# Kernel optimization log

Measured on AMD Instinct MI355X. Metric: run time of the kernel, lower is better.

Reference implementation:

```python
import jax, jax.numpy as jnp
import numpy as np

IN_CH = 256
QK_CH = IN_CH // 8  # 32

def setup_inputs() -> dict:
    key = jax.random.key(0)
    ks = jax.random.split(key, 7)
    x = jax.random.normal(ks[0], (4, IN_CH, 64, 64), dtype=jnp.float32)
    s_in = 1.0 / np.sqrt(IN_CH)
    # 1x1 conv weights stored as [out_ch, in_ch]; biases [out_ch]
    Wq = jax.random.uniform(ks[1], (QK_CH, IN_CH), jnp.float32, -s_in, s_in)
    bq = jax.random.uniform(ks[2], (QK_CH,), jnp.float32, -s_in, s_in)
    Wk = jax.random.uniform(ks[3], (QK_CH, IN_CH), jnp.float32, -s_in, s_in)
    bk = jax.random.uniform(ks[4], (QK_CH,), jnp.float32, -s_in, s_in)
    Wv = jax.random.uniform(ks[5], (IN_CH, IN_CH), jnp.float32, -s_in, s_in)
    bv = jax.random.uniform(ks[6], (IN_CH,), jnp.float32, -s_in, s_in)
    return {"x": x, "Wq": Wq, "bq": bq, "Wk": Wk, "bk": bk, "Wv": Wv, "bv": bv}

def reference(x, Wq, bq, Wk, bk, Wv, bv):
    n, c, h, w = x.shape
    xf = x.reshape(n, c, h * w)  # [n, c, hw]
    # 1x1 convs == per-position channel matmuls
    q = jnp.einsum('oc,ncs->nos', Wq, xf) + bq[None, :, None]  # [n, c/8, hw]
    k = jnp.einsum('oc,ncs->nos', Wk, xf) + bk[None, :, None]  # [n, c/8, hw]
    v = jnp.einsum('oc,ncs->nos', Wv, xf) + bv[None, :, None]  # [n, c,  hw]
    # energy[n, i, j] = <q[:, i], k[:, j]>  (no scaling, as in original)
    energy = jnp.einsum('nci,ncj->nij', q, k)  # [n, hw, hw]
    attention = jax.nn.softmax(energy, axis=-1)
    # out[n, c, i] = sum_j v[n, c, j] * attention[n, i, j]
    out = jnp.einsum('ncj,nij->nci', v, attention)
    return out.reshape(n, c, h, w)
```

## Files before the change

kernel.cpp:

```cpp
#include <hip/hip_runtime.h>
#include <hip/hip_bf16.h>
#include <stdint.h>
#include <stddef.h>

typedef unsigned short u16;
typedef unsigned int   u32;
typedef __attribute__((ext_vector_type(8))) short bf16x8;
typedef __attribute__((ext_vector_type(4))) float f32x4;

#define LOG2E   1.44269504f
#define EXP_OFF 23.0831206f

static __device__ __forceinline__ float bf2f(u16 v) {
    u32 u = ((u32)v) << 16; float f; __builtin_memcpy(&f, &u, 4); return f;
}
static __device__ __forceinline__ u16 f2bf(float f) {
    u32 u; __builtin_memcpy(&u, &f, 4);
    u32 r = (u + 0x7fffu + ((u >> 16) & 1u)) >> 16; return (u16)r;
}
static __device__ __forceinline__ float as_f(u32 u) { float f; __builtin_memcpy(&f, &u, 4); return f; }
static __device__ __forceinline__ u32   as_u(float f) { u32 u; __builtin_memcpy(&u, &f, 4); return u; }

static __device__ __forceinline__ int detect_f32_wave0(const void* x, int t) {
    const u32* xw = (const u32*)x;
    int bad = 0;
    #pragma unroll
    for (int k = 0; k < 4; ++k) {
        u32 wv = xw[(t << 2) + k];
        int e = (wv >> 7) & 0xff;
        bad += (e >= 160);
    }
    unsigned long long m = __ballot(bad > 0);
    return (__popcll(m) >= 8) ? 1 : 0;
}


__global__ __launch_bounds__(256) void qkv_proj_kernel(
    const void* __restrict__ x,
    const void* __restrict__ Wq, const void* __restrict__ bq,
    const void* __restrict__ Wk, const void* __restrict__ bk,
    const void* __restrict__ Wv, const void* __restrict__ bv,
    u16* __restrict__ qws, u16* __restrict__ kws, u16* __restrict__ vws,
    int n_off)
{
    __shared__ float Ws[32][68];
    __shared__ float Xs[32][68];
    __shared__ int dtf;

    const int t   = threadIdx.x;
    const int it  = blockIdx.x;
    const int ot  = blockIdx.y;
    const int n_w = blockIdx.z;
    const int n_g = n_off + n_w;
    const int i0  = it << 6;
    const int tx  = t & 15;
    const int ty  = t >> 4;

    if (t < 64) { int f = detect_f32_wave0(x, t); if (t == 0) dtf = f; }
    __syncthreads();
    const bool isf32 = (dtf != 0);

    float acc[4][4];
    #pragma unroll
    for (int a = 0; a < 4; ++a)
        #pragma unroll
        for (int b = 0; b < 4; ++b) acc[a][b] = 0.f;

    const int o_st   = t & 63;
    const int kk0    = (t >> 6) << 3;
    const int och_st = (ot << 6) + o_st;
    int wsel, wrow;
    if (och_st < 32)      { wsel = 0; wrow = och_st; }
    else if (och_st < 64) { wsel = 1; wrow = och_st - 32; }
    else                  { wsel = 2; wrow = och_st - 64; }
    const void* wbase = (wsel == 0) ? Wq : (wsel == 1) ? Wk : Wv;

    for (int c0 = 0; c0 < 256; c0 += 32) {
        if (isf32) {
            const float* wf = (const float*)wbase + wrow * 256 + c0 + kk0;
            #pragma unroll
            for (int k8 = 0; k8 < 8; ++k8) Ws[kk0 + k8][o_st] = wf[k8];
            const float* xf = (const float*)x;
            #pragma unroll
            for (int v = 0; v < 2; ++v) {
                int g  = t + (v << 8);
                int kk = g >> 4;
                int ii = (g & 15) << 2;
                float4 x4 = *(const float4*)(xf +
                    (((size_t)(n_g * 256 + c0 + kk)) << 12) + i0 + ii);
                Xs[kk][ii + 0] = x4.x; Xs[kk][ii + 1] = x4.y;
                Xs[kk][ii + 2] = x4.z; Xs[kk][ii + 3] = x4.w;
            }
        } else {
            const u16* wh = (const u16*)wbase + wrow * 256 + c0 + kk0;
            #pragma unroll
            for (int k8 = 0; k8 < 8; ++k8) Ws[kk0 + k8][o_st] = bf2f(wh[k8]);
            const u16* xh = (const u16*)x;
            #pragma unroll
            for (int v = 0; v < 2; ++v) {
                int g  = t + (v << 8);
                int kk = g >> 4;
                int ii = (g & 15) << 2;
                ushort4 u4 = *(const ushort4*)(xh +
                    (((size_t)(n_g * 256 + c0 + kk)) << 12) + i0 + ii);
                Xs[kk][ii + 0] = bf2f(u4.x); Xs[kk][ii + 1] = bf2f(u4.y);
                Xs[kk][ii + 2] = bf2f(u4.z); Xs[kk][ii + 3] = bf2f(u4.w);
            }
        }
        __syncthreads();

        #pragma unroll
        for (int kk = 0; kk < 32; ++kk) {
            float4 a4 = *(const float4*)&Ws[kk][ty << 2];
            float4 b4 = *(const float4*)&Xs[kk][tx << 2];
            float av[4] = {a4.x, a4.y, a4.z, a4.w};
            float bw[4] = {b4.x, b4.y, b4.z, b4.w};
            #pragma unroll
            for (int a = 0; a < 4; ++a)
                #pragma unroll
                for (int b = 0; b < 4; ++b)
                    acc[a][b] += av[a] * bw[b];
        }
        __syncthreads();
    }

    #pragma unroll
    for (int a = 0; a < 4; ++a) {
        int och = (ot << 6) + (ty << 2) + a;
        float bias;
        if (isf32) {
            if (och < 32)      bias = ((const float*)bq)[och];
            else if (och < 64) bias = ((const float*)bk)[och - 32];
            else               bias = ((const float*)bv)[och - 64];
        } else {
            if (och < 32)      bias = bf2f(((const u16*)bq)[och]);
            else if (och < 64) bias = bf2f(((const u16*)bk)[och - 32]);
            else               bias = bf2f(((const u16*)bv)[och - 64]);
        }
        if (och < 32) {
            #pragma unroll
            for (int b = 0; b < 4; ++b) {
                int i = i0 + (tx << 2) + b;
                qws[(((size_t)(n_w << 12) + i) << 5) + och] =
                    f2bf((acc[a][b] + bias) * LOG2E);
            }
        } else if (och < 64) {
            #pragma unroll
            for (int b = 0; b < 4; ++b) {
                int i = i0 + (tx << 2) + b;
                kws[(((size_t)(n_w << 12) + i) << 5) + (och - 32)] =
                    f2bf(acc[a][b] + bias);
            }
        } else {
            const int c = och - 64;
            const int i = i0 + (tx << 2);
            ushort4 h;
            h.x = f2bf(acc[a][0] + bias);
            h.y = f2bf(acc[a][1] + bias);
            h.z = f2bf(acc[a][2] + bias);
            h.w = f2bf(acc[a][3] + bias);
            const size_t addr = ((size_t)n_w << 20)
                + ((size_t)(c >> 4) << 16)
                + ((size_t)(i >> 5) << 9)
                + (size_t)((((((i & 31) >> 3) << 4) + (c & 15)) << 3) + (i & 7));
            *(ushort4*)(vws + addr) = h;
        }
    }
}

__global__ __launch_bounds__(1024) void flash_mfma6(
    const u16* __restrict__ qws, const u16* __restrict__ kws,
    const u16* __restrict__ vws, void* __restrict__ out,
    const void* __restrict__ x, int n_off, int nshift)
{
    __shared__ __align__(16) char arena[17920];
    __shared__ __align__(16) float lS[64];
    __shared__ int dtf;
    u16*   PsA  = (u16*)arena;
    float* Dbuf = (float*)arena;

    const int t    = threadIdx.x;
    const int lane = t & 63;
    const int w    = t >> 6;
    const int n16  = lane & 15;
    const int quad = lane >> 4;
    const int bid  = blockIdx.x;
    const int n_w  = bid & ((1 << nshift) - 1);
    const int qt   = bid >> nshift;
    const int n_g  = n_off + n_w;
    const int i0   = qt << 6;

    if (t < 64) {
        int f = detect_f32_wave0(x, t);
        if (t == 0) dtf = f;
        lS[t] = 0.f;
    }

    const u16* qb = qws + (((size_t)n_w) << 17);
    const u16* kb = kws + (((size_t)n_w) << 17);
    const u16* vb = vws + (((size_t)n_w) << 20);

    const int qsub_s = w & 3;
    const int jsub   = w >> 2;
    const int cq = w & 7;
    const int jq = w >> 3;

    const bf16x8 qfrag =
        *(const bf16x8*)(qb + ((size_t)(i0 + (qsub_s << 4) + n16) << 5) + (quad << 3));

    f32x4 acc[4][2];
    #pragma unroll
    for (int a = 0; a < 4; ++a)
        #pragma unroll
        for (int b = 0; b < 2; ++b) acc[a][b] = (f32x4){0.f, 0.f, 0.f, 0.f};
    float lp[4] = {0.f, 0.f, 0.f, 0.f};

    const int jcol = (jsub << 4) + n16;
    const int j8   = jcol >> 3;
    const int jlo  = jcol & 7;
    const int ksw  = (jq << 2) + quad;

    const u16* vfp0 = vb + ((size_t)(cq << 1) << 16) + ((size_t)jq << 9)
                         + ((size_t)((quad << 4) + n16) << 3);
    const u16* vfp1 = vfp0 + 65536;

    bf16x8 kreg, vf0, vf1;

    kreg = *(const bf16x8*)(kb + ((size_t)((jsub << 4) + n16) << 5) + (quad << 3));
    {
        u16* Ps = PsA;
        const f32x4 z = {0.f, 0.f, 0.f, 0.f};
        f32x4 s = __builtin_amdgcn_mfma_f32_16x16x32_bf16(qfrag, kreg, z, 0, 0, 0);
        #pragma unroll
        for (int r = 0; r < 4; ++r) {
            const int qrow = (qsub_s << 4) + (quad << 2) + r;
            float p = exp2f(s[r] - EXP_OFF);
            u32 u = as_u(p) & 0xffff0000u;
            lp[r] += as_f(u);
            Ps[qrow * 64 + ((j8 ^ (qrow & 7)) << 3) + jlo] = (u16)(u >> 16);
        }
        kreg = *(const bf16x8*)(kb + ((size_t)(64 + (jsub << 4) + n16) << 5) + (quad << 3));
        vf0 = *(const bf16x8*)(vfp0);
        vf1 = *(const bf16x8*)(vfp1);
    }
    __syncthreads();

    for (int tile = 1; tile < 64; ++tile) {
        const int par  = tile & 1;
        u16* Psc = PsA + (par << 12);
        u16* Psp = PsA + ((par ^ 1) << 12);

        bf16x8 pa[4];
        #pragma unroll
        for (int qs = 0; qs < 4; ++qs) {
            const int qrow = (qs << 4) + n16;
            pa[qs] = *(const bf16x8*)&Psp[qrow * 64 + ((ksw ^ (qrow & 7)) << 3)];
        }
        #pragma unroll
        for (int qs = 0; qs < 4; ++qs) {
            acc[qs][0] = __builtin_amdgcn_mfma_f32_16x16x32_bf16(pa[qs], vf0, acc[qs][0], 0, 0, 0);
            acc[qs][1] = __builtin_amdgcn_mfma_f32_16x16x32_bf16(pa[qs], vf1, acc[qs][1], 0, 0, 0);
        }

        vf0 = *(const bf16x8*)(vfp0 + ((size_t)tile << 10));
        vf1 = *(const bf16x8*)(vfp1 + ((size_t)tile << 10));

        const f32x4 z = {0.f, 0.f, 0.f, 0.f};
        f32x4 s = __builtin_amdgcn_mfma_f32_16x16x32_bf16(qfrag, kreg, z, 0, 0, 0);
        #pragma unroll
        for (int r = 0; r < 4; ++r) {
            const int qrow = (qsub_s << 4) + (quad << 2) + r;
            float p = exp2f(s[r] - EXP_OFF);
            u32 u = as_u(p) & 0xffff0000u;
            lp[r] += as_f(u);
            Psc[qrow * 64 + ((j8 ^ (qrow & 7)) << 3) + jlo] = (u16)(u >> 16);
        }

        if (tile < 63) {
            const int j0n = (tile + 1) << 6;
            kreg = *(const bf16x8*)(kb + ((size_t)(j0n + (jsub << 4) + n16) << 5)
                                    + (quad << 3));
        }
        __syncthreads();
    }

    {
        u16* Psp = PsA + (1 << 12);
        bf16x8 pa[4];
        #pragma unroll
        for (int qs = 0; qs < 4; ++qs) {
            const int qrow = (qs << 4) + n16;
            pa[qs] = *(const bf16x8*)&Psp[qrow * 64 + ((ksw ^ (qrow & 7)) << 3)];
        }
        #pragma unroll
        for (int qs = 0; qs < 4; ++qs) {
            acc[qs][0] = __builtin_amdgcn_mfma_f32_16x16x32_bf16(pa[qs], vf0, acc[qs][0], 0, 0, 0);
            acc[qs][1] = __builtin_amdgcn_mfma_f32_16x16x32_bf16(pa[qs], vf1, acc[qs][1], 0, 0, 0);
        }
    }

    #pragma unroll
    for (int r = 0; r < 4; ++r) {
        lp[r] += __shfl_xor(lp[r], 1);
        lp[r] += __shfl_xor(lp[r], 2);
        lp[r] += __shfl_xor(lp[r], 4);
        lp[r] += __shfl_xor(lp[r], 8);
    }
    if (n16 == 0) {
        #pragma unroll
        for (int r = 0; r < 4; ++r)
            atomicAdd(&lS[(qsub_s << 4) + (quad << 2) + r], lp[r]);
    }
    __syncthreads();
    if (t < 64) lS[t] = 1.0f / lS[t];
    const bool isf32 = (dtf != 0);

    for (int chunk = 0; chunk < 4; ++chunk) {
        __syncthreads();
        if (jq == 1 && (cq >> 1) == chunk) {
            #pragma unroll
            for (int qs = 0; qs < 4; ++qs)
                #pragma unroll
                for (int cs = 0; cs < 2; ++cs)
                    *(f32x4*)&Dbuf[(((cq & 1) << 5) + (cs << 4) + n16) * 68 +
                                   (qs << 4) + (quad << 2)] = acc[qs][cs];
        }
        __syncthreads();
        if (jq == 0 && (cq >> 1) == chunk) {
            #pragma unroll
            for (int qs = 0; qs < 4; ++qs)
                #pragma unroll
                for (int cs = 0; cs < 2; ++cs) {
                    float* p = &Dbuf[(((cq & 1) << 5) + (cs << 4) + n16) * 68 +
                                     (qs << 4) + (quad << 2)];
                    f32x4 d = *(f32x4*)p;
                    d += acc[qs][cs];
                    *(f32x4*)p = d;
                }
        }
        __syncthreads();
        const int c_l = t >> 4;
        const int qg  = (t & 15) << 2;
        float4 d  = *(float4*)&Dbuf[c_l * 68 + qg];
        float4 rl = *(float4*)&lS[qg];
        const int c_glob = (chunk << 6) + c_l;
        const size_t ob = (((size_t)(n_g * 256 + c_glob)) << 12) + i0 + qg;
        if (isf32) {
            float4 o = make_float4(d.x * rl.x, d.y * rl.y, d.z * rl.z, d.w * rl.w);
            *(float4*)((float*)out + ob) = o;
        } else {
            union { uint2 v; u16 h[4]; } o;
            o.h[0] = f2bf(d.x * rl.x);
            o.h[1] = f2bf(d.y * rl.y);
            o.h[2] = f2bf(d.z * rl.z);
            o.h[3] = f2bf(d.w * rl.w);
            *(uint2*)((u16*)out + ob) = o.v;
        }
    }
}

extern "C" void kernel_launch(void* const* d_in, const int* in_sizes, int n_in,
                              void* d_out, int out_size, void* d_ws, size_t ws_size,
                              hipStream_t stream)
{
    const void* x  = d_in[0];
    const void* Wq = d_in[1];
    const void* bq = d_in[2];
    const void* Wk = d_in[3];
    const void* bk = d_in[4];
    const void* Wv = d_in[5];
    const void* bv = d_in[6];

    const size_t full_need = (size_t)(4u * 4096u) * (32 + 32 + 256) * 2;
    if (ws_size >= full_need) {
        u16* qws = (u16*)d_ws;
        u16* kws = qws + (size_t)4 * 4096 * 32;
        u16* vws = kws + (size_t)4 * 4096 * 32;
        qkv_proj_kernel<<<dim3(64, 5, 4), dim3(256), 0, stream>>>(
            x, Wq, bq, Wk, bk, Wv, bv, qws, kws, vws, 0);
        flash_mfma6<<<dim3(256), dim3(1024), 0, stream>>>(
            qws, kws, vws, d_out, x, 0, 2);
    } else {
        u16* qws = (u16*)d_ws;
        u16* kws = qws + (size_t)4096 * 32;
        u16* vws = kws + (size_t)4096 * 32;
        for (int n = 0; n < 4; ++n) {
            qkv_proj_kernel<<<dim3(64, 5, 1), dim3(256), 0, stream>>>(
                x, Wq, bq, Wk, bk, Wv, bv, qws, kws, vws, n);
            flash_mfma6<<<dim3(64), dim3(1024), 0, stream>>>(
                qws, kws, vws, d_out, x, n, 0);
        }
    }
}
```

Before: 160.2 us.

## Rewrite QKV projection to use bf16 MFMA with swizzled LDS weights

Replaces the fp32 SIMT tiled GEMM in the QKV projection with a kernel that stages a 64x256 weight slab in LDS as bf16 (XOR-swizzled) and computes with 16x16x32 bf16 MFMA instructions. Activations are loaded straight from global memory per lane, converted to bf16 and prefetched one step ahead. The grid becomes 1D with the batch index in the low bits so that consecutive blocks cover different batches. Rounding inputs to bf16 before the projection lowers precision, and the strided per-lane global loads of x may coalesce less well.

```diff
diff --git a/kernel.cpp b/kernel.cpp
--- a/kernel.cpp
+++ b/kernel.cpp
@@ -35,134 +35,148 @@
 }
 
 
-__global__ __launch_bounds__(256) void qkv_proj_kernel(
+__global__ __launch_bounds__(256) void qkv_proj_mfma(
     const void* __restrict__ x,
     const void* __restrict__ Wq, const void* __restrict__ bq,
     const void* __restrict__ Wk, const void* __restrict__ bk,
     const void* __restrict__ Wv, const void* __restrict__ bv,
     u16* __restrict__ qws, u16* __restrict__ kws, u16* __restrict__ vws,
-    int n_off)
+    int n_off, int nshiftp)
 {
-    __shared__ float Ws[32][68];
-    __shared__ float Xs[32][68];
+    __shared__ u16 Wl[64 * 256];
     __shared__ int dtf;
 
-    const int t   = threadIdx.x;
-    const int it  = blockIdx.x;
-    const int ot  = blockIdx.y;
-    const int n_w = blockIdx.z;
-    const int n_g = n_off + n_w;
-    const int i0  = it << 6;
-    const int tx  = t & 15;
-    const int ty  = t >> 4;
+    const int t    = threadIdx.x;
+    const int bid  = blockIdx.x;
+    const int n_w  = bid & ((1 << nshiftp) - 1);
+    const int rest = bid >> nshiftp;
+    const int g    = rest % 5;
+    const int it   = rest / 5;
+    const int n_g  = n_off + n_w;
+    const int i0   = it << 6;
 
     if (t < 64) { int f = detect_f32_wave0(x, t); if (t == 0) dtf = f; }
     __syncthreads();
     const bool isf32 = (dtf != 0);
 
-    float acc[4][4];
     #pragma unroll
-    for (int a = 0; a < 4; ++a)
-        #pragma unroll
-        for (int b = 0; b < 4; ++b) acc[a][b] = 0.f;
-
-    const int o_st   = t & 63;
-    const int kk0    = (t >> 6) << 3;
-    const int och_st = (ot << 6) + o_st;
-    int wsel, wrow;
-    if (och_st < 32)      { wsel = 0; wrow = och_st; }
-    else if (och_st < 64) { wsel = 1; wrow = och_st - 32; }
-    else                  { wsel = 2; wrow = och_st - 64; }
-    const void* wbase = (wsel == 0) ? Wq : (wsel == 1) ? Wk : Wv;
-
-    for (int c0 = 0; c0 < 256; c0 += 32) {
+    for (int k = 0; k < 16; ++k) {
+        int idx  = t + (k << 8);
+        int row  = idx >> 6;
+        int col4 = (idx & 63) << 2;
+        const void* src; int srow;
+        if (g == 0) {
+            if (row < 32) { src = Wq; srow = row; }
+            else          { src = Wk; srow = row - 32; }
+        } else { src = Wv; srow = ((g - 1) << 6) + row; }
+        ushort4 h;
         if (isf32) {
-            const float* wf = (const float*)wbase + wrow * 256 + c0 + kk0;
-            #pragma unroll
-            for (int k8 = 0; k8 < 8; ++k8) Ws[kk0 + k8][o_st] = wf[k8];
-            const float* xf = (const float*)x;
-            #pragma unroll
-            for (int v = 0; v < 2; ++v) {
-                int g  = t + (v << 8);
-                int kk = g >> 4;
-                int ii = (g & 15) << 2;
-                float4 x4 = *(const float4*)(xf +
-                    (((size_t)(n_g * 256 + c0 + kk)) << 12) + i0 + ii);
-                Xs[kk][ii + 0] = x4.x; Xs[kk][ii + 1] = x4.y;
-                Xs[kk][ii + 2] = x4.z; Xs[kk][ii + 3] = x4.w;
+            float4 wv = *((const float4*)((const float*)src + srow * 256 + col4));
+            h.x = f2bf(wv.x); h.y = f2bf(wv.y); h.z = f2bf(wv.z); h.w = f2bf(wv.w);
+        } else {
+            h = *((const ushort4*)((const u16*)src + srow * 256 + col4));
+        }
+        *(ushort4*)&Wl[(row << 8) + (col4 ^ ((row & 7) << 3))] = h;
+    }
+    __syncthreads();
+
+    const int lane = t & 63;
+    const int w    = t >> 6;
+    const int n16  = lane & 15;
+    const int quad = lane >> 4;
+    const int i_b  = i0 + (w << 4);
+    const int i    = i_b + n16;
+    const int swz  = (n16 & 7) << 3;
+
+    f32x4 acc[4];
+    #pragma unroll
+    for (int f = 0; f < 4; ++f) acc[f] = (f32x4){0.f, 0.f, 0.f, 0.f};
+
+    if (isf32) {
+        const float* xp = (const float*)x
+            + (((size_t)(n_g * 256 + (quad << 3))) << 12) + i;
+        float af[8];
+        #pragma unroll
+        for (int e = 0; e < 8; ++e) af[e] = xp[(size_t)e << 12];
+        #pragma unroll
+        for (int c8 = 0; c8 < 8; ++c8) {
+            bf16x8 a;
+            #pragma unroll
+            for (int e = 0; e < 8; ++e) a[e] = (short)f2bf(af[e]);
+            if (c8 < 7) {
+                const float* xn = xp + (((size_t)(c8 + 1) << 5) << 12);
+                #pragma unroll
+                for (int e = 0; e < 8; ++e) af[e] = xn[(size_t)e << 12];
             }
-        } else {
-            const u16* wh = (const u16*)wbase + wrow * 256 + c0 + kk0;
-            #pragma unroll
-            for (int k8 = 0; k8 < 8; ++k8) Ws[kk0 + k8][o_st] = bf2f(wh[k8]);
-            const u16* xh = (const u16*)x;
-            #pragma unroll
-            for (int v = 0; v < 2; ++v) {
-                int g  = t + (v << 8);
-                int kk = g >> 4;
-                int ii = (g & 15) << 2;
-                ushort4 u4 = *(const ushort4*)(xh +
-                    (((size_t)(n_g * 256 + c0 + kk)) << 12) + i0 + ii);
-                Xs[kk][ii + 0] = bf2f(u4.x); Xs[kk][ii + 1] = bf2f(u4.y);
-                Xs[kk][ii + 2] = bf2f(u4.z); Xs[kk][ii + 3] = bf2f(u4.w);
+            const int c0 = c8 << 5;
+            #pragma unroll
+            for (int f = 0; f < 4; ++f) {
+                const int brow = (f << 4) + n16;
+                bf16x8 b = *(const bf16x8*)
+                    &Wl[(brow << 8) + ((c0 + (quad << 3)) ^ swz)];
+                acc[f] = __builtin_amdgcn_mfma_f32_16x16x32_bf16(a, b, acc[f], 0, 0, 0);
             }
         }
-        __syncthreads();
-
-        #pragma unroll
-        for (int kk = 0; kk < 32; ++kk) {
-            float4 a4 = *(const float4*)&Ws[kk][ty << 2];
-            float4 b4 = *(const float4*)&Xs[kk][tx << 2];
-            float av[4] = {a4.x, a4.y, a4.z, a4.w};
-            float bw[4] = {b4.x, b4.y, b4.z, b4.w};
-            #pragma unroll
-            for (int a = 0; a < 4; ++a)
+    } else {
+        const u16* xp = (const u16*)x
+            + (((size_t)(n_g * 256 + (quad << 3))) << 12) + i;
+        u16 af[8];
+        #pragma unroll
+        for (int e = 0; e < 8; ++e) af[e] = xp[(size_t)e << 12];
+        #pragma unroll
+        for (int c8 = 0; c8 < 8; ++c8) {
+            bf16x8 a;
+            #pragma unroll
+            for (int e = 0; e < 8; ++e) a[e] = (short)af[e];
+            if (c8 < 7) {
+                const u16* xn = xp + (((size_t)(c8 + 1) << 5) << 12);
                 #pragma unroll
-                for (int b = 0; b < 4; ++b)
-                    acc[a][b] += av[a] * bw[b];
-        }
-        __syncthreads();
-    }
-
-    #pragma unroll
-    for (int a = 0; a < 4; ++a) {
-        int och = (ot << 6) + (ty << 2) + a;
-        float bias;
-        if (isf32) {
-            if (och < 32)      bias = ((const float*)bq)[och];
-            else if (och < 64) bias = ((const float*)bk)[och - 32];
-            else               bias = ((const float*)bv)[och - 64];
-        } else {
-            if (och < 32)      bias = bf2f(((const u16*)bq)[och]);
-            else if (och < 64) bias = bf2f(((const u16*)bk)[och - 32]);
-            else               bias = bf2f(((const u16*)bv)[och - 64]);
-        }
-        if (och < 32) {
-            #pragma unroll
-            for (int b = 0; b < 4; ++b) {
-                int i = i0 + (tx << 2) + b;
-                qws[(((size_t)(n_w << 12) + i) << 5) + och] =
-                    f2bf((acc[a][b] + bias) * LOG2E);
+                for (int e = 0; e < 8; ++e) af[e] = xn[(size_t)e << 12];
             }
-        } else if (och < 64) {
-            #pragma unroll
-            for (int b = 0; b < 4; ++b) {
-                int i = i0 + (tx << 2) + b;
-                kws[(((size_t)(n_w << 12) + i) << 5) + (och - 32)] =
-                    f2bf(acc[a][b] + bias);
+            const int c0 = c8 << 5;
+            #pragma unroll
+            for (int f = 0; f < 4; ++f) {
+                const int brow = (f << 4) + n16;
+                bf16x8 b = *(const bf16x8*)
+                    &Wl[(brow << 8) + ((c0 + (quad << 3)) ^ swz)];
+                acc[f] = __builtin_amdgcn_mfma_f32_16x16x32_bf16(a, b, acc[f], 0, 0, 0);
             }
-        } else {
-            const int c = och - 64;
-            const int i = i0 + (tx << 2);
+        }
+    }
+
+    if (g == 0) {
+        #pragma unroll
+        for (int f = 0; f < 4; ++f) {
+            const int ol   = (f << 4) + n16;
+            const bool isq = (ol < 32);
+            const int och  = isq ? ol : (ol - 32);
+            float bias;
+            if (isf32) bias = ((const float*)(isq ? bq : bk))[och];
+            else       bias = bf2f(((const u16*)(isq ? bq : bk))[och]);
+            u16* dst = (isq ? qws : kws) + (((size_t)n_w) << 17) + och;
+            const float scale = isq ? LOG2E : 1.0f;
+            #pragma unroll
+            for (int r = 0; r < 4; ++r) {
+                const int ii = i_b + (quad << 2) + r;
+                dst[(size_t)ii << 5] = f2bf((acc[f][r] + bias) * scale);
+            }
+        }
+    } else {
+        #pragma unroll
+        for (int f = 0; f < 4; ++f) {
+            const int c = ((g - 1) << 6) + (f << 4) + n16;
+            float bias = isf32 ? ((const float*)bv)[c]
+                               : bf2f(((const u16*)bv)[c]);
+            const int i4 = i_b + (quad << 2);
             ushort4 h;
-            h.x = f2bf(acc[a][0] + bias);
-            h.y = f2bf(acc[a][1] + bias);
-            h.z = f2bf(acc[a][2] + bias);
-            h.w = f2bf(acc[a][3] + bias);
+            h.x = f2bf(acc[f][0] + bias);
+            h.y = f2bf(acc[f][1] + bias);
+            h.z = f2bf(acc[f][2] + bias);
+            h.w = f2bf(acc[f][3] + bias);
             const size_t addr = ((size_t)n_w << 20)
                 + ((size_t)(c >> 4) << 16)
-                + ((size_t)(i >> 5) << 9)
-                + (size_t)((((((i & 31) >> 3) << 4) + (c & 15)) << 3) + (i & 7));
+                + ((size_t)(i4 >> 5) << 9)
+                + (size_t)((((((i4 & 31) >> 3) << 4) + (c & 15)) << 3) + (i4 & 7));
             *(ushort4*)(vws + addr) = h;
         }
     }
@@ -376,8 +390,8 @@
         u16* qws = (u16*)d_ws;
         u16* kws = qws + (size_t)4 * 4096 * 32;
         u16* vws = kws + (size_t)4 * 4096 * 32;
-        qkv_proj_kernel<<<dim3(64, 5, 4), dim3(256), 0, stream>>>(
-            x, Wq, bq, Wk, bk, Wv, bv, qws, kws, vws, 0);
+        qkv_proj_mfma<<<dim3(1280), dim3(256), 0, stream>>>(
+            x, Wq, bq, Wk, bk, Wv, bv, qws, kws, vws, 0, 2);
         flash_mfma6<<<dim3(256), dim3(1024), 0, stream>>>(
             qws, kws, vws, d_out, x, 0, 2);
     } else {
@@ -385,8 +399,8 @@
         u16* kws = qws + (size_t)4096 * 32;
         u16* vws = kws + (size_t)4096 * 32;
         for (int n = 0; n < 4; ++n) {
-            qkv_proj_kernel<<<dim3(64, 5, 1), dim3(256), 0, stream>>>(
-                x, Wq, bq, Wk, bk, Wv, bv, qws, kws, vws, n);
+            qkv_proj_mfma<<<dim3(320), dim3(256), 0, stream>>>(
+                x, Wq, bq, Wk, bk, Wv, bv, qws, kws, vws, n, 0);
             flash_mfma6<<<dim3(64), dim3(1024), 0, stream>>>(
                 qws, kws, vws, d_out, x, n, 0);
         }
```

New measurement: 144.5 us. -9.8%, faster.
